# Optimization experiments

Hardware: AMD Instinct MI355X
Metric: run time of the kernel (lower is better)

## Reference

```python
import jax, jax.numpy as jnp
import numpy as np

B, C, H, W = 8, 512, 64, 64
D = C // 8  # 64

def setup_inputs() -> dict:
    key = jax.random.key(0)
    ks = jax.random.split(key, 10)
    s = 0.02
    return {
        "x":  jax.random.normal(ks[0], (B, C, H, W), dtype=jnp.float32),
        "Wq": jax.random.normal(ks[1], (D, C), dtype=jnp.float32) * s,
        "bq": jnp.zeros((D,), dtype=jnp.float32),
        "Wk": jax.random.normal(ks[2], (D, C), dtype=jnp.float32) * s,
        "bk": jnp.zeros((D,), dtype=jnp.float32),
        "Wv": jax.random.normal(ks[3], (D, C), dtype=jnp.float32) * s,
        "bv": jnp.zeros((D,), dtype=jnp.float32),
        "Wo": jax.random.normal(ks[4], (C, D), dtype=jnp.float32) * s,
        "bo": jnp.zeros((C,), dtype=jnp.float32),
        "gamma": jnp.full((1,), 0.5, dtype=jnp.float32),
    }

def reference(x, Wq, bq, Wk, bk, Wv, bv, Wo, bo, gamma):
    b, c, h, w = x.shape
    n = h * w
    xf = x.reshape(b, c, n)                                   # (B, C, N)
    # 1x1 convs == channel matmuls (spectral_norm only reparametrizes the weight)
    q = jnp.einsum('dc,bcn->bnd', Wq, xf) + bq                # (B, N, D)
    k = jnp.einsum('dc,bcn->bdn', Wk, xf) + bk[:, None]       # (B, D, N)
    v = jnp.einsum('dc,bcn->bdn', Wv, xf) + bv[:, None]       # (B, D, N)
    # unscaled scores, softmax over key index (last dim)
    attn = jax.nn.softmax(jnp.einsum('bnd,bdm->bnm', q, k), axis=-1)  # (B, N, N)
    out = jnp.einsum('bdm,bnm->bdn', v, attn)                 # (B, D, N)
    out = jnp.einsum('cd,bdn->bcn', Wo, out) + bo[:, None]    # (B, C, N)
    return (out * gamma + xf).reshape(b, c, h, w)
```

## Files before the change

kernel.cpp:

```cpp
#include <hip/hip_runtime.h>
#include <hip/hip_bf16.h>

#define DEVFN __device__ __forceinline__

typedef __bf16 bf16x8 __attribute__((ext_vector_type(8)));
typedef float f32x4 __attribute__((ext_vector_type(4)));
typedef float float4_t __attribute__((ext_vector_type(4)));
typedef unsigned short ushort8_t __attribute__((ext_vector_type(8)));
typedef unsigned short ushort4_t __attribute__((ext_vector_type(4)));
typedef unsigned int uint4_t __attribute__((ext_vector_type(4)));

constexpr int Bd = 8, Cd = 512, Nd = 4096, Dd = 64;

DEVFN unsigned short f2bf(float f) {
    union { float f; unsigned int u; } v; v.f = f;
    unsigned int r = (v.u + 0x7FFFu + ((v.u >> 16) & 1u)) >> 16;
    return (unsigned short)r;
}

DEVFN unsigned int pack2(float a, float b) {
    __hip_bfloat162 h = __float22bfloat162_rn(make_float2(a, b));
    union { __hip_bfloat162 h; unsigned int u; } c; c.h = h;
    return c.u;
}

DEVFN bf16x8 ld_bf8(const unsigned short* p) {
    ushort8_t u = *(const ushort8_t*)p;
    return __builtin_bit_cast(bf16x8, u);
}

DEVFN f32x4 mfma16(bf16x8 a, bf16x8 b, f32x4 c) {
    return __builtin_amdgcn_mfma_f32_16x16x32_bf16(a, b, c, 0, 0, 0);
}

__global__ __launch_bounds__(256) void k_cvtw(
    const float* __restrict__ Wq, const float* __restrict__ Wk,
    const float* __restrict__ Wv, const float* __restrict__ Wo,
    unsigned short* __restrict__ w4)
{
    int i = blockIdx.x * 256 + threadIdx.x;
    w4[i]          = f2bf(Wq[i]);
    w4[32768 + i]  = f2bf(Wk[i]);
    w4[65536 + i]  = f2bf(Wv[i]);
    w4[98304 + i]  = f2bf(Wo[i]);
}

__global__ __launch_bounds__(256, 1) void k_qkv(
    const float* __restrict__ x,
    const unsigned short* __restrict__ wq,
    const unsigned short* __restrict__ wk,
    const unsigned short* __restrict__ wv,
    const float* __restrict__ bq, const float* __restrict__ bk, const float* __restrict__ bv,
    unsigned short* __restrict__ q_nd, unsigned short* __restrict__ k_nd,
    unsigned short* __restrict__ v_dn)
{
    const int b   = blockIdx.y;
    const int n0  = blockIdx.x * 64;
    const int tid = threadIdx.x, wid = tid >> 6, l = tid & 63;
    const int lo  = l & 15, hi = l >> 4;
    const float* xb = x + (size_t)b * Cd * Nd;

    __shared__ unsigned short smem[2][64][72];

    f32x4 acc[12] = {};

    const int scr = tid >> 4;
    const int snf = tid & 15;
    float4_t xr[4];

    auto gload = [&](int t) {
        const int c0 = t * 64;
        #pragma unroll
        for (int p = 0; p < 4; ++p)
            xr[p] = *(const float4_t*)(xb + (size_t)(c0 + p*16 + scr) * Nd + n0 + snf*4);
    };
    auto dswrite = [&](int buf) {
        #pragma unroll
        for (int p = 0; p < 4; ++p)
            #pragma unroll
            for (int i = 0; i < 4; ++i)
                smem[buf][snf*4 + i][p*16 + scr] = f2bf(xr[p][i]);
    };
    auto compute = [&](int buf, int t) {
        const int c0 = t * 64;
        #pragma unroll
        for (int kk = 0; kk < 2; ++kk) {
            bf16x8 af = ld_bf8(&smem[buf][wid*16 + lo][kk*32 + hi*8]);
            #pragma unroll
            for (int j = 0; j < 12; ++j) {
                const unsigned short* wm = (j < 4) ? wq : (j < 8) ? wk : wv;
                const int d0 = (j & 3) * 16;
                bf16x8 bf = ld_bf8(wm + (d0 + lo) * Cd + c0 + kk*32 + hi*8);
                acc[j] = mfma16(af, bf, acc[j]);
            }
        }
    };

    gload(0);
    dswrite(0);
    __syncthreads();
    for (int t = 0; t < 8; ++t) {
        const int cur = t & 1;
        if (t + 1 < 8) gload(t + 1);
        __builtin_amdgcn_sched_barrier(0);
        compute(cur, t);
        if (t + 1 < 8) dswrite(cur ^ 1);
        __syncthreads();
    }

    unsigned short* tl = &smem[0][wid*16][0];
    #pragma unroll
    for (int m = 0; m < 2; ++m) {
        const float* bias = m ? bk : bq;
        #pragma unroll
        for (int jj = 0; jj < 4; ++jj) {
            const float bia = bias[jj*16 + lo];
            #pragma unroll
            for (int r = 0; r < 4; ++r)
                tl[(hi*4 + r) * 72 + jj*16 + lo] = f2bf(acc[m*4 + jj][r] + bia);
        }
        asm volatile("" ::: "memory");
        const int row = l >> 2, dg = l & 3;
        ushort8_t a0 = *(const ushort8_t*)&tl[row*72 + dg*16];
        ushort8_t a1 = *(const ushort8_t*)&tl[row*72 + dg*16 + 8];
        unsigned short* dst = (m ? k_nd : q_nd)
            + ((size_t)b * Nd + n0 + wid*16 + row) * 64 + dg*16;
        *(ushort8_t*)dst = a0; *(ushort8_t*)(dst + 8) = a1;
        asm volatile("" ::: "memory");
    }

    #pragma unroll
    for (int jj = 0; jj < 4; ++jj) {
        const float bia = bv[jj*16 + lo];
        #pragma unroll
        for (int r = 0; r < 4; ++r)
            smem[1][jj*16 + lo][wid*16 + hi*4 + r] = f2bf(acc[8 + jj][r] + bia);
    }
    __syncthreads();
    {
        const int d = tid >> 2, ng = tid & 3;
        ushort8_t a0 = *(const ushort8_t*)&smem[1][d][ng*16];
        ushort8_t a1 = *(const ushort8_t*)&smem[1][d][ng*16 + 8];
        unsigned short* dst = v_dn + ((size_t)b * Dd + d) * Nd + n0 + ng*16;
        *(ushort8_t*)dst = a0; *(ushort8_t*)(dst + 8) = a1;
    }
}

__global__ __launch_bounds__(256, 2) void k_attn(
    const unsigned short* __restrict__ q_nd,
    const unsigned short* __restrict__ k_nd,
    const unsigned short* __restrict__ v_dn,
    unsigned short* __restrict__ o_nd)
{
    const int bid = blockIdx.x;
    const int b   = bid & 7;
    const int n0  = (bid >> 3) * 64;
    const int tid = threadIdx.x, wid = tid >> 6, l = tid & 63;
    const int lo  = l & 15, hi = l >> 4;
    const int lsw = lo & 7;
    const int qh  = wid >> 1;
    const int kh  = wid & 1;
    const int wk0 = kh * 32;

    __shared__ unsigned short k_tiles[2][64 * 64];
    __shared__ unsigned short v_tiles[2][64 * 64];
    __shared__ float red_acc[2][2][4][256];
    __shared__ float red_l[2][2][16];

    const unsigned short* qb = q_nd + (size_t)b * Nd * Dd;
    const unsigned short* kb = k_nd + (size_t)b * Nd * Dd;
    const unsigned short* vb = v_dn + (size_t)b * Dd * Nd;

    bf16x8 aq[2][2];
    #pragma unroll
    for (int qs = 0; qs < 2; ++qs)
        #pragma unroll
        for (int kc = 0; kc < 2; ++kc)
            aq[qs][kc] = ld_bf8(qb + (size_t)(n0 + qh*32 + qs*16 + lo) * 64 + kc*32 + hi*8);

    f32x4 acc[2][4] = {};
    float l_p[2] = {0.f, 0.f};

    const int sr = tid >> 3, ss = tid & 7;
    const int kwsl = (ss ^ (sr & 7)) * 8;
    const int vkh = ss >> 2, vsl = ss & 3, vms = vsl >> 1;
    const int vg0 = vkh * 4 + ((2 * vsl) & 3);
    const int vg1 = vkh * 4 + ((2 * vsl + 1) & 3);
    const int vsw = sr & 7;
    ushort8_t kr0, kr1, vr0, vr1;

    auto gload = [&](int t) {
        const size_t m1 = (size_t)t * 64;
        kr0 = *(const ushort8_t*)(kb + (m1 + sr) * 64 + ss * 8);
        kr1 = *(const ushort8_t*)(kb + (m1 + 32 + sr) * 64 + ss * 8);
        vr0 = *(const ushort8_t*)(vb + (size_t)sr * Nd + m1 + ss * 8);
        vr1 = *(const ushort8_t*)(vb + (size_t)(32 + sr) * Nd + m1 + ss * 8);
    };
    auto dswrite = [&](int buf) {
        unsigned short* kt = k_tiles[buf];
        unsigned short* vt = v_tiles[buf];
        *(ushort8_t*)(kt + sr * 64 + kwsl)        = kr0;
        *(ushort8_t*)(kt + (32 + sr) * 64 + kwsl) = kr1;
        ushort4_t a0 = __builtin_shufflevector(vr0, vr0, 0, 1, 2, 3);
        ushort4_t a1 = __builtin_shufflevector(vr0, vr0, 4, 5, 6, 7);
        ushort4_t b0 = __builtin_shufflevector(vr1, vr1, 0, 1, 2, 3);
        ushort4_t b1 = __builtin_shufflevector(vr1, vr1, 4, 5, 6, 7);
        *(ushort4_t*)(vt + sr * 64 + (vg0 ^ vsw) * 8 + vms * 4)        = a0;
        *(ushort4_t*)(vt + sr * 64 + (vg1 ^ vsw) * 8 + vms * 4)        = a1;
        *(ushort4_t*)(vt + (32 + sr) * 64 + (vg0 ^ vsw) * 8 + vms * 4) = b0;
        *(ushort4_t*)(vt + (32 + sr) * 64 + (vg1 ^ vsw) * 8 + vms * 4) = b1;
    };

    auto compute = [&](int buf) {
        const unsigned short* kt = k_tiles[buf];
        const unsigned short* vt = v_tiles[buf];
        f32x4 s[2][2] = {};
        #pragma unroll
        for (int ms = 0; ms < 2; ++ms) {
            #pragma unroll
            for (int kc = 0; kc < 2; ++kc) {
                bf16x8 kf = ld_bf8(kt + (wk0 + ms*16 + lo) * 64 + (((kc*4 + hi) ^ lsw) * 8));
                #pragma unroll
                for (int qs = 0; qs < 2; ++qs)
                    s[qs][ms] = mfma16(kf, aq[qs][kc], s[qs][ms]);
            }
        }
        bf16x8 vf[4];
        #pragma unroll
        for (int ds = 0; ds < 4; ++ds)
            vf[ds] = ld_bf8(vt + (ds*16 + lo) * 64 + (((kh*4 + hi) ^ lsw) * 8));
        #pragma unroll
        for (int qs = 0; qs < 2; ++qs) {
            float p[2][4];
            #pragma unroll
            for (int ms = 0; ms < 2; ++ms)
                #pragma unroll
                for (int r = 0; r < 4; ++r)
                    p[ms][r] = __expf(s[qs][ms][r]);
            l_p[qs] += ((p[0][0] + p[0][1]) + (p[0][2] + p[0][3]))
                     + ((p[1][0] + p[1][1]) + (p[1][2] + p[1][3]));
            uint4_t w;
            w[0] = pack2(p[0][0], p[0][1]);
            w[1] = pack2(p[0][2], p[0][3]);
            w[2] = pack2(p[1][0], p[1][1]);
            w[3] = pack2(p[1][2], p[1][3]);
            bf16x8 apf = __builtin_bit_cast(bf16x8, w);
            #pragma unroll
            for (int ds = 0; ds < 4; ++ds)
                acc[qs][ds] = mfma16(apf, vf[ds], acc[qs][ds]);
        }
    };

    constexpr int NT = Nd / 64;
    gload(0);
    dswrite(0);
    __syncthreads();
    for (int t = 0; t < NT; ++t) {
        const int cur = t & 1;
        if (t + 1 < NT) gload(t + 1);
        __builtin_amdgcn_sched_barrier(0);
        compute(cur);
        if (t + 1 < NT) dswrite(cur ^ 1);
        __syncthreads();
    }

    float lh[2];
    #pragma unroll
    for (int qs = 0; qs < 2; ++qs) {
        float ps = l_p[qs];
        ps += __shfl_xor(ps, 16, 64);
        ps += __shfl_xor(ps, 32, 64);
        lh[qs] = ps;
    }
    if (kh == 1) {
        #pragma unroll
        for (int qs = 0; qs < 2; ++qs) {
            #pragma unroll
            for (int ds = 0; ds < 4; ++ds)
                *(f32x4*)&red_acc[qh][qs][ds][l * 4] = acc[qs][ds];
            red_l[qh][qs][lo] = lh[qs];
        }
    }
    __syncthreads();
    if (kh == 0) {
        #pragma unroll
        for (int qs = 0; qs < 2; ++qs) {
            #pragma unroll
            for (int ds = 0; ds < 4; ++ds)
                acc[qs][ds] += *(const f32x4*)&red_acc[qh][qs][ds][l * 4];
            float l_tot = lh[qs] + red_l[qh][qs][lo];
            #pragma unroll
            for (int r = 0; r < 4; ++r) {
                float lq = __shfl(l_tot, hi * 4 + r, 16);
                float rl = 1.0f / lq;
                #pragma unroll
                for (int ds = 0; ds < 4; ++ds) {
                    float o = acc[qs][ds][r] * rl;
                    o_nd[((size_t)b * Nd + n0 + qh*32 + qs*16 + hi*4 + r) * 64 + ds*16 + lo] = f2bf(o);
                }
            }
        }
    }
}

__global__ __launch_bounds__(256) void k_oproj(
    const unsigned short* __restrict__ o_nd,
    const unsigned short* __restrict__ wo,
    const float* __restrict__ bo,
    const float* __restrict__ gamma,
    const float* __restrict__ x,
    float* __restrict__ out)
{
    const int b   = blockIdx.y;
    const int n0  = blockIdx.x * 64;
    const int tid = threadIdx.x, wid = tid >> 6, l = tid & 63;
    const int lo  = l & 15, hi = l >> 4;
    const int n0w = n0 + wid * 16;
    const float g = gamma[0];

    bf16x8 ao[2];
    #pragma unroll
    for (int kc = 0; kc < 2; ++kc)
        ao[kc] = ld_bf8(o_nd + ((size_t)b * Nd + n0w + lo) * 64 + kc*32 + hi*8);

    for (int ct = 0; ct < 32; ++ct) {
        f32x4 acc = {};
        #pragma unroll
        for (int kc = 0; kc < 2; ++kc) {
            bf16x8 bw = ld_bf8(wo + (ct*16 + lo) * 64 + kc*32 + hi*8);
            acc = mfma16(ao[kc], bw, acc);
        }
        const int c = ct*16 + lo;
        const float bc = bo[c];
        const size_t base = ((size_t)b * Cd + c) * Nd + n0w + hi*4;
        float4_t xv = *(const float4_t*)(x + base);
        float4_t ov;
        #pragma unroll
        for (int r = 0; r < 4; ++r) ov[r] = g * (acc[r] + bc) + xv[r];
        *(float4_t*)(out + base) = ov;
    }
}

extern "C" void kernel_launch(void* const* d_in, const int* in_sizes, int n_in,
                              void* d_out, int out_size, void* d_ws, size_t ws_size,
                              hipStream_t stream) {
    (void)in_sizes; (void)n_in; (void)out_size; (void)ws_size;
    const float* x  = (const float*)d_in[0];
    const float* Wq = (const float*)d_in[1];
    const float* bq = (const float*)d_in[2];
    const float* Wk = (const float*)d_in[3];
    const float* bk = (const float*)d_in[4];
    const float* Wv = (const float*)d_in[5];
    const float* bv = (const float*)d_in[6];
    const float* Wo = (const float*)d_in[7];
    const float* bo = (const float*)d_in[8];
    const float* gm = (const float*)d_in[9];
    float* out = (float*)d_out;

    unsigned short* w4   = (unsigned short*)d_ws;
    unsigned short* q_nd = w4 + 131072;
    unsigned short* k_nd = q_nd + (size_t)Bd * Nd * Dd;
    unsigned short* v_dn = k_nd + (size_t)Bd * Nd * Dd;
    unsigned short* o_nd = v_dn + (size_t)Bd * Nd * Dd;

    k_cvtw<<<128, 256, 0, stream>>>(Wq, Wk, Wv, Wo, w4);
    dim3 gq(Nd / 64, Bd);
    k_qkv<<<gq, 256, 0, stream>>>(x, w4, w4 + 32768, w4 + 65536, bq, bk, bv, q_nd, k_nd, v_dn);
    k_attn<<<512, 256, 0, stream>>>(q_nd, k_nd, v_dn, o_nd);
    dim3 g1(Nd / 64, Bd);
    k_oproj<<<g1, 256, 0, stream>>>(o_nd, w4 + 98304, bo, gm, x, out);
}
```

Before: 152.2 us.

## Shrink QKV projection tiles to 32 tokens and prefetch x two stages ahead

Restructures the QKV projection kernel so each block covers 32 tokens with 128 threads (two waves), which doubles the grid and allows two blocks per CU. The x loads are now double-buffered in registers (A/B sets), so global loads for stage t+2 are issued while stage t is computed. The V transpose epilogue is rewritten for the smaller tile. The intent is more parallelism and deeper latency hiding for this memory-bound projection, at the cost of more register pressure and reloading the weights from global memory twice as often per token.

```diff
diff --git a/kernel.cpp b/kernel.cpp
--- a/kernel.cpp
+++ b/kernel.cpp
@@ -45,7 +45,7 @@
     w4[98304 + i]  = f2bf(Wo[i]);
 }
 
-__global__ __launch_bounds__(256, 1) void k_qkv(
+__global__ __launch_bounds__(128, 2) void k_qkv(
     const float* __restrict__ x,
     const unsigned short* __restrict__ wq,
     const unsigned short* __restrict__ wk,
@@ -55,31 +55,44 @@
     unsigned short* __restrict__ v_dn)
 {
     const int b   = blockIdx.y;
-    const int n0  = blockIdx.x * 64;
+    const int n0  = blockIdx.x * 32;
     const int tid = threadIdx.x, wid = tid >> 6, l = tid & 63;
     const int lo  = l & 15, hi = l >> 4;
     const float* xb = x + (size_t)b * Cd * Nd;
 
-    __shared__ unsigned short smem[2][64][72];
+    __shared__ unsigned short smem[2][32][72];
 
     f32x4 acc[12] = {};
 
-    const int scr = tid >> 4;
-    const int snf = tid & 15;
-    float4_t xr[4];
-
-    auto gload = [&](int t) {
+    const int scr = tid >> 3;
+    const int snf = tid & 7;
+    float4_t xrA[4], xrB[4];
+
+    auto gloadA = [&](int t) {
         const int c0 = t * 64;
         #pragma unroll
         for (int p = 0; p < 4; ++p)
-            xr[p] = *(const float4_t*)(xb + (size_t)(c0 + p*16 + scr) * Nd + n0 + snf*4);
-    };
-    auto dswrite = [&](int buf) {
+            xrA[p] = *(const float4_t*)(xb + (size_t)(c0 + p*16 + scr) * Nd + n0 + snf*4);
+    };
+    auto gloadB = [&](int t) {
+        const int c0 = t * 64;
         #pragma unroll
         for (int p = 0; p < 4; ++p)
+            xrB[p] = *(const float4_t*)(xb + (size_t)(c0 + p*16 + scr) * Nd + n0 + snf*4);
+    };
+    auto dswriteA = [&](int buf) {
+        #pragma unroll
+        for (int p = 0; p < 4; ++p)
             #pragma unroll
             for (int i = 0; i < 4; ++i)
-                smem[buf][snf*4 + i][p*16 + scr] = f2bf(xr[p][i]);
+                smem[buf][snf*4 + i][p*16 + scr] = f2bf(xrA[p][i]);
+    };
+    auto dswriteB = [&](int buf) {
+        #pragma unroll
+        for (int p = 0; p < 4; ++p)
+            #pragma unroll
+            for (int i = 0; i < 4; ++i)
+                smem[buf][snf*4 + i][p*16 + scr] = f2bf(xrB[p][i]);
     };
     auto compute = [&](int buf, int t) {
         const int c0 = t * 64;
@@ -96,19 +109,24 @@
         }
     };
 
-    gload(0);
-    dswrite(0);
+    gloadA(0);
+    dswriteA(0);
+    gloadB(1);
     __syncthreads();
-    for (int t = 0; t < 8; ++t) {
-        const int cur = t & 1;
-        if (t + 1 < 8) gload(t + 1);
+    for (int t = 0; t < 8; t += 2) {
+        if (t + 2 < 8) gloadA(t + 2);
         __builtin_amdgcn_sched_barrier(0);
-        compute(cur, t);
-        if (t + 1 < 8) dswrite(cur ^ 1);
+        compute(0, t);
+        dswriteB(1);
         __syncthreads();
-    }
-
-    unsigned short* tl = &smem[0][wid*16][0];
+        if (t + 3 < 8) gloadB(t + 3);
+        __builtin_amdgcn_sched_barrier(0);
+        compute(1, t + 1);
+        if (t + 2 < 8) dswriteA(0);
+        __syncthreads();
+    }
+
+    unsigned short* tl = &smem[1][wid*16][0];
     #pragma unroll
     for (int m = 0; m < 2; ++m) {
         const float* bias = m ? bk : bq;
@@ -129,20 +147,22 @@
         asm volatile("" ::: "memory");
     }
 
+    unsigned short* vt = &smem[0][0][0];
     #pragma unroll
     for (int jj = 0; jj < 4; ++jj) {
         const float bia = bv[jj*16 + lo];
         #pragma unroll
         for (int r = 0; r < 4; ++r)
-            smem[1][jj*16 + lo][wid*16 + hi*4 + r] = f2bf(acc[8 + jj][r] + bia);
+            vt[(jj*16 + lo) * 36 + wid*16 + hi*4 + r] = f2bf(acc[8 + jj][r] + bia);
     }
     __syncthreads();
-    {
-        const int d = tid >> 2, ng = tid & 3;
-        ushort8_t a0 = *(const ushort8_t*)&smem[1][d][ng*16];
-        ushort8_t a1 = *(const ushort8_t*)&smem[1][d][ng*16 + 8];
-        unsigned short* dst = v_dn + ((size_t)b * Dd + d) * Nd + n0 + ng*16;
-        *(ushort8_t*)dst = a0; *(ushort8_t*)(dst + 8) = a1;
+    #pragma unroll
+    for (int p = 0; p < 2; ++p) {
+        const int d = p*32 + (tid >> 2), ng = tid & 3;
+        ushort4_t a0 = *(const ushort4_t*)&vt[d*36 + ng*8];
+        ushort4_t a1 = *(const ushort4_t*)&vt[d*36 + ng*8 + 4];
+        unsigned short* dst = v_dn + ((size_t)b * Dd + d) * Nd + n0 + ng*8;
+        *(ushort4_t*)dst = a0; *(ushort4_t*)(dst + 4) = a1;
     }
 }
 
@@ -364,8 +384,8 @@
     unsigned short* o_nd = v_dn + (size_t)Bd * Nd * Dd;
 
     k_cvtw<<<128, 256, 0, stream>>>(Wq, Wk, Wv, Wo, w4);
-    dim3 gq(Nd / 64, Bd);
-    k_qkv<<<gq, 256, 0, stream>>>(x, w4, w4 + 32768, w4 + 65536, bq, bk, bv, q_nd, k_nd, v_dn);
+    dim3 gq(Nd / 32, Bd);
+    k_qkv<<<gq, 128, 0, stream>>>(x, w4, w4 + 32768, w4 + 65536, bq, bk, bv, q_nd, k_nd, v_dn);
     k_attn<<<512, 256, 0, stream>>>(q_nd, k_nd, v_dn, o_nd);
     dim3 g1(Nd / 64, Bd);
     k_oproj<<<g1, 256, 0, stream>>>(o_nd, w4 + 98304, bo, gm, x, out);
```

Result: faster. 144.1 us (-5.3%).
